# Kernel tuning notes

Hardware: AMD Instinct MI355X
Metric: run time of the kernel (lower is better)

## Reference

```python
import jax, jax.numpy as jnp
import numpy as np

N_NODES = 50000
N_EDGES = 800000
D_IN = 16
HID = 128
D_OUT = 4
N_LAYERS = 3
LN_EPS = 1e-5


def _layer_norm(h, g, b):
    mu = jnp.mean(h, axis=-1, keepdims=True)
    var = jnp.mean(jnp.square(h - mu), axis=-1, keepdims=True)
    return (h - mu) * jax.lax.rsqrt(var + LN_EPS) * g + b


def setup_inputs() -> dict:
    key = jax.random.key(0)
    ks = jax.random.split(key, 8)
    x = jax.random.normal(ks[0], (N_NODES, D_IN), jnp.float32)
    edge_index = jax.random.randint(ks[1], (2, N_EDGES), 0, N_NODES, jnp.int32)
    W_in = jax.random.normal(ks[2], (D_IN, HID), jnp.float32) / np.sqrt(D_IN)
    b_in = jnp.zeros((HID,), jnp.float32)
    Wl = jax.random.normal(ks[3], (N_LAYERS, HID, HID), jnp.float32) / np.sqrt(HID)
    bl = jnp.zeros((N_LAYERS, HID), jnp.float32)
    Wr = jax.random.normal(ks[4], (N_LAYERS, HID, HID), jnp.float32) / np.sqrt(HID)
    ln_g = jnp.ones((N_LAYERS, HID), jnp.float32)
    ln_b = jnp.zeros((N_LAYERS, HID), jnp.float32)
    W_out = jax.random.normal(ks[5], (HID, D_OUT), jnp.float32) / np.sqrt(HID)
    b_out = jnp.zeros((D_OUT,), jnp.float32)
    return {
        "x": x, "edge_index": edge_index,
        "W_in": W_in, "b_in": b_in,
        "Wl": Wl, "bl": bl, "Wr": Wr,
        "ln_g": ln_g, "ln_b": ln_b,
        "W_out": W_out, "b_out": b_out,
    }


def reference(x, edge_index, W_in, b_in, Wl, bl, Wr, ln_g, ln_b, W_out, b_out):
    # Eval mode: DropEdge and dropout are identity.
    src, dst = edge_index[0], edge_index[1]
    n = x.shape[0]
    e = edge_index.shape[1]
    # Mean-aggregation normalizer over incoming edges (PyG SAGEConv aggr='mean').
    deg = jax.ops.segment_sum(jnp.ones((e,), x.dtype), dst, num_segments=n)
    inv_deg = 1.0 / jnp.maximum(deg, 1.0)  # [N]

    h = x @ W_in + b_in  # [N, HID]
    for i in range(N_LAYERS):
        hn = _layer_norm(h, ln_g[i], ln_b[i])
        # gather source features [E, HID], scatter-sum into destinations, then mean
        agg = jax.ops.segment_sum(hn[src], dst, num_segments=n) * inv_deg[:, None]
        conv = agg @ Wl[i] + bl[i] + hn @ Wr[i]  # lin_l(mean) + lin_r(self)
        h = jax.nn.relu(h + conv)  # residual + relu
    return h @ W_out + b_out  # [N, D_OUT]
```

## Files before the change

kernel.cpp:

```cpp
#include <hip/hip_runtime.h>

#define N_NODES 50000
#define N_EDGES 800000
#define D_IN 16
#define HID 128
#define D_OUT 4
#define N_LAYERS 3
#define LN_EPS 1e-5f
#define ELL_CAP 48
#define NBUCK 196
#define BCAP 5120
#define SENT N_NODES
#define NBP 256
#define EPB (N_EDGES / NBP)
#define NB_W    (N_LAYERS * 128)
#define NB_IN   (N_NODES / 16)

typedef __attribute__((ext_vector_type(8))) short bf16x8;
typedef __attribute__((ext_vector_type(4))) float f32x4;
typedef __attribute__((ext_vector_type(2))) float f32x2;

__device__ __forceinline__ unsigned short f2bf(float f) {
    union { float f; unsigned int u; } a; a.f = f;
    unsigned int r = a.u + 0x7fffu + ((a.u >> 16) & 1u);
    return (unsigned short)(r >> 16);
}
__device__ __forceinline__ unsigned int pack2(float x, float y) {
    return (unsigned int)f2bf(x) | ((unsigned int)f2bf(y) << 16);
}
__device__ __forceinline__ float bf2f(unsigned short u) {
    union { unsigned int u; float f; } c; c.u = (unsigned int)u << 16; return c.f;
}

__global__ __launch_bounds__(256) void prep_kernel(
        const int* __restrict__ src, const int* __restrict__ dst,
        int* __restrict__ gbase, unsigned int* __restrict__ part,
        const float* __restrict__ Wl, const float* __restrict__ Wr,
        unsigned short* __restrict__ BT,
        const float* __restrict__ x, const float* __restrict__ W_in,
        const float* __restrict__ b_in,
        const float* __restrict__ g0, const float* __restrict__ bb0,
        unsigned short* __restrict__ h, unsigned short* __restrict__ hnb,
        unsigned char* __restrict__ a8) {
    __shared__ int cnt[NBUCK];
    int b = blockIdx.x, t = threadIdx.x;
    if (b < NBP) {
        if (t < NBUCK) cnt[t] = 0;
        __syncthreads();
        int e0 = b * EPB;
        for (int i = t; i < EPB; i += 256)
            atomicAdd(&cnt[dst[e0 + i] >> 8], 1);
        __syncthreads();
        int mybase = 0;
        if (t < NBUCK) mybase = atomicAdd(&gbase[t], cnt[t]);
        __syncthreads();
        if (t < NBUCK) cnt[t] = mybase;
        __syncthreads();
        for (int i = t; i < EPB; i += 256) {
            int d = dst[e0 + i];
            int bk = d >> 8;
            int pos = atomicAdd(&cnt[bk], 1);
            if (pos < BCAP)
                part[(size_t)bk * BCAP + pos] =
                    (unsigned int)src[e0 + i] | ((unsigned int)(d & 255) << 16);
        }
        return;
    }
    b -= NBP;
    if (b < NB_W) {
        int i = b >> 7, n = b & 127;
        float v = (t < 128) ? Wl[((size_t)i * 128 + t) * 128 + n]
                            : Wr[((size_t)i * 128 + (t - 128)) * 128 + n];
        BT[((size_t)i * 128 + n) * 256 + t] = f2bf(v);
        return;
    }
    b -= NB_W;
    int l = t & 15, nq = t >> 4;
    int node = b * 16 + nq;
    if (node >= N_NODES) return;
    int qb = (t & 63) & ~15;
    int j0 = l * 8;
    float xv = x[(size_t)node * D_IN + l];
    float acc[8];
    {
        float4 b0 = *(const float4*)(b_in + j0);
        float4 b1 = *(const float4*)(b_in + j0 + 4);
        acc[0] = b0.x; acc[1] = b0.y; acc[2] = b0.z; acc[3] = b0.w;
        acc[4] = b1.x; acc[5] = b1.y; acc[6] = b1.z; acc[7] = b1.w;
    }
    #pragma unroll
    for (int k = 0; k < D_IN; ++k) {
        float xk = __shfl(xv, qb + k, 64);
        float4 w0 = *(const float4*)(W_in + k * HID + j0);
        float4 w1 = *(const float4*)(W_in + k * HID + j0 + 4);
        acc[0] += xk * w0.x; acc[1] += xk * w0.y; acc[2] += xk * w0.z; acc[3] += xk * w0.w;
        acc[4] += xk * w1.x; acc[5] += xk * w1.y; acc[6] += xk * w1.z; acc[7] += xk * w1.w;
    }
    unsigned int hw[4];
    hw[0] = pack2(acc[0], acc[1]); hw[1] = pack2(acc[2], acc[3]);
    hw[2] = pack2(acc[4], acc[5]); hw[3] = pack2(acc[6], acc[7]);
    ((uint4*)h)[(size_t)node * 16 + l] = *(uint4*)hw;
    float s = ((acc[0] + acc[1]) + (acc[2] + acc[3])) + ((acc[4] + acc[5]) + (acc[6] + acc[7]));
    #pragma unroll
    for (int o = 1; o < 16; o <<= 1) s += __shfl_xor(s, o, 64);
    float mu = s * (1.0f / HID);
    float qs = 0.f;
    float d[8];
    #pragma unroll
    for (int j = 0; j < 8; ++j) { d[j] = acc[j] - mu; qs += d[j] * d[j]; }
    #pragma unroll
    for (int o = 1; o < 16; o <<= 1) qs += __shfl_xor(qs, o, 64);
    float rstd = rsqrtf(qs * (1.0f / HID) + LN_EPS);
    float4 gv0 = *(const float4*)(g0 + j0), gv1 = *(const float4*)(g0 + j0 + 4);
    float4 bv0 = *(const float4*)(bb0 + j0), bv1 = *(const float4*)(bb0 + j0 + 4);
    float hv[8];
    hv[0] = d[0] * rstd * gv0.x + bv0.x; hv[1] = d[1] * rstd * gv0.y + bv0.y;
    hv[2] = d[2] * rstd * gv0.z + bv0.z; hv[3] = d[3] * rstd * gv0.w + bv0.w;
    hv[4] = d[4] * rstd * gv1.x + bv1.x; hv[5] = d[5] * rstd * gv1.y + bv1.y;
    hv[6] = d[6] * rstd * gv1.z + bv1.z; hv[7] = d[7] * rstd * gv1.w + bv1.w;
    unsigned int nw[4];
    nw[0] = pack2(hv[0], hv[1]); nw[1] = pack2(hv[2], hv[3]);
    nw[2] = pack2(hv[4], hv[5]); nw[3] = pack2(hv[6], hv[7]);
    ((uint4*)hnb)[(size_t)node * 16 + l] = *(uint4*)nw;
    int r0 = __builtin_amdgcn_cvt_pk_fp8_f32(hv[0], hv[1], 0, false);
    r0     = __builtin_amdgcn_cvt_pk_fp8_f32(hv[2], hv[3], r0, true);
    int r1 = __builtin_amdgcn_cvt_pk_fp8_f32(hv[4], hv[5], 0, false);
    r1     = __builtin_amdgcn_cvt_pk_fp8_f32(hv[6], hv[7], r1, true);
    uint2 o8; o8.x = (unsigned int)r0; o8.y = (unsigned int)r1;
    *(uint2*)(a8 + (size_t)node * 256 + 128 + (size_t)l * 8) = o8;
}

__global__ __launch_bounds__(256) void ell_kernel(
        const unsigned int* __restrict__ part, const int* __restrict__ gbase,
        unsigned short* __restrict__ ell, int* __restrict__ cursor,
        unsigned char* __restrict__ a8) {
    __shared__ int cnt[256];
    int b = blockIdx.x, t = threadIdx.x;
    cnt[t] = 0;
    __syncthreads();
    int total = gbase[b];
    if (total > BCAP) total = BCAP;
    int n0 = b * 256;
    for (int i = t; i < total; i += 256) {
        unsigned int rec = part[(size_t)b * BCAP + i];
        int dl = rec >> 16;
        int slot = atomicAdd(&cnt[dl], 1);
        if (slot < ELL_CAP)
            ell[(size_t)(n0 + dl) * ELL_CAP + slot] = (unsigned short)(rec & 0xffff);
    }
    __syncthreads();
    int n = n0 + t;
    if (n < N_NODES) {
        int c = cnt[t];
        cursor[n] = c;
        int cap = c < ELL_CAP ? c : ELL_CAP;
        int padto = (cap + 7) & ~7;
        for (int s2 = cap; s2 < padto; ++s2)
            ell[(size_t)n * ELL_CAP + s2] = (unsigned short)SENT;
    }
    if (b == 0 && t < 32)
        ((unsigned int*)(a8 + (size_t)SENT * 256 + 128))[t] = 0u;
}

__global__ __launch_bounds__(256) void gather_kernel(
        const int* __restrict__ cursor, const unsigned short* __restrict__ ell,
        unsigned char* __restrict__ a8) {
    int tid = threadIdx.x;
    int node = blockIdx.x * 16 + (tid >> 4);
    if (node >= N_NODES) return;
    int l = tid & 15;
    int qbase = (tid & 63) & ~15;
    const uint2* base = (const uint2*)a8;
    const unsigned short* row = ell + (size_t)node * ELL_CAP;
    int cnt = cursor[node];
    int mc = cnt < ELL_CAP ? cnt : ELL_CAP;
    int mp = (mc + 7) & ~7;
    float a[8];
    #pragma unroll
    for (int j = 0; j < 8; ++j) a[j] = 0.f;
    for (int i = 0; i < mp; i += 8) {
        int sv = row[i + (l & 7)];
        uint2 vv[8];
        #pragma unroll
        for (int j = 0; j < 8; ++j) {
            int s = __shfl(sv, qbase + j, 64);
            vv[j] = base[(size_t)s * 32 + 16 + l];
        }
        #pragma unroll
        for (int j = 0; j < 8; ++j) {
            f32x2 p0 = __builtin_amdgcn_cvt_pk_f32_fp8((int)vv[j].x, false);
            f32x2 p1 = __builtin_amdgcn_cvt_pk_f32_fp8((int)vv[j].x, true);
            f32x2 p2 = __builtin_amdgcn_cvt_pk_f32_fp8((int)vv[j].y, false);
            f32x2 p3 = __builtin_amdgcn_cvt_pk_f32_fp8((int)vv[j].y, true);
            a[0] += p0.x; a[1] += p0.y; a[2] += p1.x; a[3] += p1.y;
            a[4] += p2.x; a[5] += p2.y; a[6] += p3.x; a[7] += p3.y;
        }
    }
    float inv = 1.0f / fmaxf((float)cnt, 1.0f);
    int r0 = __builtin_amdgcn_cvt_pk_fp8_f32(a[0] * inv, a[1] * inv, 0, false);
    r0     = __builtin_amdgcn_cvt_pk_fp8_f32(a[2] * inv, a[3] * inv, r0, true);
    int r1 = __builtin_amdgcn_cvt_pk_fp8_f32(a[4] * inv, a[5] * inv, 0, false);
    r1     = __builtin_amdgcn_cvt_pk_fp8_f32(a[6] * inv, a[7] * inv, r1, true);
    uint2 o; o.x = (unsigned int)r0; o.y = (unsigned int)r1;
    ((uint2*)a8)[(size_t)node * 32 + l] = o;
}

__global__ __launch_bounds__(256) void conv_mfma_kernel(
        const unsigned short* __restrict__ hres, const unsigned char* __restrict__ a8c,
        unsigned char* __restrict__ a8, unsigned short* __restrict__ hnb,
        const unsigned short* __restrict__ BT, const float* __restrict__ bl,
        const float* __restrict__ lng, const float* __restrict__ lnb,
        unsigned short* __restrict__ h,
        const float* __restrict__ Wout, const float* __restrict__ bout,
        float* __restrict__ out, int mode) {
    __shared__ unsigned short s_ab[2 * 128 * 64];
    unsigned short* s_a = s_ab;
    unsigned short* s_b = s_ab + 128 * 64;
    __shared__ float s_bl[128], s_g[128], s_bb[128];
    __shared__ float s_wo[512];
    __shared__ float s_bo[4];
    int tid = threadIdx.x;
    int n0 = blockIdx.x * 128;
    if (tid < 128) {
        s_bl[tid] = bl[tid];
        s_g[tid]  = (mode == 1) ? lng[tid] : 0.f;
        s_bb[tid] = (mode == 1) ? lnb[tid] : 0.f;
    }
    if (mode == 2) {
        s_wo[tid]       = Wout[tid];
        s_wo[tid + 256] = Wout[tid + 256];
        if (tid < 4) s_bo[tid] = bout[tid];
    }
    int w = tid >> 6, lane = tid & 63;
    int q = lane >> 4, c0 = lane & 15;

    f32x4 acc[2][8];
    #pragma unroll
    for (int rt = 0; rt < 2; ++rt)
        #pragma unroll
        for (int ct = 0; ct < 8; ++ct) acc[rt][ct] = (f32x4){0.f, 0.f, 0.f, 0.f};

    for (int kc = 0; kc < 4; ++kc) {
        if (kc) __syncthreads();
        if (kc < 2) {
            #pragma unroll
            for (int p = 0; p < 2; ++p) {
                int f = p * 256 + tid;
                int row = f >> 2, j = f & 3;
                uint4 v = {0u, 0u, 0u, 0u};
                int node = n0 + row;
                if (node < N_NODES)
                    v = *(const uint4*)(a8c + (size_t)node * 256 + kc * 64 + j * 16);
                f32x2 p0 = __builtin_amdgcn_cvt_pk_f32_fp8((int)v.x, false);
                f32x2 p1 = __builtin_amdgcn_cvt_pk_f32_fp8((int)v.x, true);
                f32x2 p2 = __builtin_amdgcn_cvt_pk_f32_fp8((int)v.y, false);
                f32x2 p3 = __builtin_amdgcn_cvt_pk_f32_fp8((int)v.y, true);
                uint4 o0;
                o0.x = pack2(p0.x, p0.y); o0.y = pack2(p1.x, p1.y);
                o0.z = pack2(p2.x, p2.y); o0.w = pack2(p3.x, p3.y);
                p0 = __builtin_amdgcn_cvt_pk_f32_fp8((int)v.z, false);
                p1 = __builtin_amdgcn_cvt_pk_f32_fp8((int)v.z, true);
                p2 = __builtin_amdgcn_cvt_pk_f32_fp8((int)v.w, false);
                p3 = __builtin_amdgcn_cvt_pk_f32_fp8((int)v.w, true);
                uint4 o1;
                o1.x = pack2(p0.x, p0.y); o1.y = pack2(p1.x, p1.y);
                o1.z = pack2(p2.x, p2.y); o1.w = pack2(p3.x, p3.y);
                int g0 = 2 * j, g1 = 2 * j + 1;
                *(uint4*)(s_a + row * 64 + (g0 ^ (row & 7)) * 8) = o0;
                *(uint4*)(s_a + row * 64 + (g1 ^ (row & 7)) * 8) = o1;
            }
        } else {
            #pragma unroll
            for (int p = 0; p < 4; ++p) {
                int f = p * 256 + tid;
                int row = f >> 3, g = f & 7;
                int pos = g ^ (row & 7);
                uint4 v = {0u, 0u, 0u, 0u};
                int node = n0 + row;
                if (node < N_NODES)
                    v = *(const uint4*)(hnb + (size_t)node * 128 + (kc - 2) * 64 + g * 8);
                *(uint4*)(s_a + row * 64 + pos * 8) = v;
            }
        }
        #pragma unroll
        for (int p = 0; p < 4; ++p) {
            int f = p * 256 + tid;
            int row = f >> 3, g = f & 7;
            int pos = g ^ (row & 7);
            uint4 v = *(const uint4*)(BT + (size_t)row * 256 + kc * 64 + g * 8);
            *(uint4*)(s_b + row * 64 + pos * 8) = v;
        }
        __syncthreads();
        #pragma unroll
        for (int ks = 0; ks < 2; ++ks) {
            int g = ks * 4 + q;
            bf16x8 af[2], bfr[8];
            #pragma unroll
            for (int rt = 0; rt < 2; ++rt) {
                int row = w * 32 + rt * 16 + c0;
                af[rt] = *(const bf16x8*)(s_a + row * 64 + (g ^ (row & 7)) * 8);
            }
            #pragma unroll
            for (int ct = 0; ct < 8; ++ct) {
                int row = ct * 16 + c0;
                bfr[ct] = *(const bf16x8*)(s_b + row * 64 + (g ^ (row & 7)) * 8);
            }
            #pragma unroll
            for (int rt = 0; rt < 2; ++rt)
                #pragma unroll
                for (int ct = 0; ct < 8; ++ct)
                    acc[rt][ct] = __builtin_amdgcn_mfma_f32_16x16x32_bf16(
                        af[rt], bfr[ct], acc[rt][ct], 0, 0, 0);
        }
    }

    if (mode == 1) {
        __syncthreads();
        unsigned short* s_out = s_ab;
        #pragma unroll
        for (int rt = 0; rt < 2; ++rt)
        #pragma unroll
        for (int reg = 0; reg < 4; ++reg) {
            int row = w * 32 + rt * 16 + q * 4 + reg;
            int nd = n0 + row;
            if (nd >= N_NODES) continue;
            #pragma unroll
            for (int ct = 0; ct < 8; ++ct) {
                int col = ct * 16 + c0;
                float v = acc[rt][ct][reg] + s_bl[col] + bf2f(hres[(size_t)nd * HID + col]);
                s_out[row * 128 + col] = f2bf(fmaxf(v, 0.f));
            }
        }
        __syncthreads();
        {
            int row = tid >> 1, half = tid & 1;
            if (n0 + row < N_NODES) {
                const uint4* sp = (const uint4*)s_ab + row * 16 + half * 8;
                uint4* gp = (uint4*)h + (size_t)(n0 + row) * 16 + half * 8;
                #pragma unroll
                for (int i = 0; i < 8; ++i) gp[i] = sp[i];
            }
        }
        __syncthreads();
        #pragma unroll
        for (int rt = 0; rt < 2; ++rt)
        #pragma unroll
        for (int reg = 0; reg < 4; ++reg) {
            int row = w * 32 + rt * 16 + q * 4 + reg;
            int nd = n0 + row;
            if (nd >= N_NODES) continue;
            float o2[8]; float s = 0.f;
            #pragma unroll
            for (int ct = 0; ct < 8; ++ct) {
                o2[ct] = bf2f(s_out[row * 128 + ct * 16 + c0]);
                s += o2[ct];
            }
            #pragma unroll
            for (int off = 1; off < 16; off <<= 1) s += __shfl_xor(s, off, 64);
            float mu = s * (1.0f / HID);
            float qs = 0.f;
            #pragma unroll
            for (int ct = 0; ct < 8; ++ct) { float d = o2[ct] - mu; qs += d * d; }
            #pragma unroll
            for (int off = 1; off < 16; off <<= 1) qs += __shfl_xor(qs, off, 64);
            float rstd = rsqrtf(qs * (1.0f / HID) + LN_EPS);
            #pragma unroll
            for (int ct = 0; ct < 8; ++ct) {
                int col = ct * 16 + c0;
                float hv = (o2[ct] - mu) * rstd * s_g[col] + s_bb[col];
                s_out[row * 128 + col] = f2bf(hv);
            }
        }
        __syncthreads();
        {
            int row = tid >> 1, half = tid & 1;
            if (n0 + row < N_NODES) {
                const uint4* sp = (const uint4*)s_ab + row * 16 + half * 8;
                uint4* gp = (uint4*)hnb + (size_t)(n0 + row) * 16 + half * 8;
                uint4 vv[8];
                #pragma unroll
                for (int i = 0; i < 8; ++i) { vv[i] = sp[i]; gp[i] = vv[i]; }
                unsigned int w8[16];
                #pragma unroll
                for (int i = 0; i < 8; ++i) {
                    const unsigned int* pu = (const unsigned int*)&vv[i];
                    #pragma unroll
                    for (int k2 = 0; k2 < 2; ++k2) {
                        unsigned int u0 = pu[2 * k2], u1 = pu[2 * k2 + 1];
                        int r = __builtin_amdgcn_cvt_pk_fp8_f32(
                            bf2f((unsigned short)(u0 & 0xffff)),
                            bf2f((unsigned short)(u0 >> 16)), 0, false);
                        r = __builtin_amdgcn_cvt_pk_fp8_f32(
                            bf2f((unsigned short)(u1 & 0xffff)),
                            bf2f((unsigned short)(u1 >> 16)), r, true);
                        w8[i * 2 + k2] = (unsigned int)r;
                    }
                }
                uint4* ap = (uint4*)(a8 + (size_t)(n0 + row) * 256 + 128 + half * 64);
                #pragma unroll
                for (int i = 0; i < 4; ++i) ap[i] = *(uint4*)&w8[i * 4];
            }
        }
    } else {
        #pragma unroll
        for (int rt = 0; rt < 2; ++rt) {
            #pragma unroll
            for (int reg = 0; reg < 4; ++reg) {
                int nd = n0 + w * 32 + rt * 16 + q * 4 + reg;
                if (nd >= N_NODES) continue;
                float od0 = 0.f, od1 = 0.f, od2 = 0.f, od3 = 0.f;
                #pragma unroll
                for (int ct = 0; ct < 8; ++ct) {
                    int col = ct * 16 + c0;
                    float v = acc[rt][ct][reg] + s_bl[col] + bf2f(hres[(size_t)nd * HID + col]);
                    v = fmaxf(v, 0.f);
                    od0 += v * s_wo[col * 4 + 0];
                    od1 += v * s_wo[col * 4 + 1];
                    od2 += v * s_wo[col * 4 + 2];
                    od3 += v * s_wo[col * 4 + 3];
                }
                #pragma unroll
                for (int off = 1; off < 16; off <<= 1) {
                    od0 += __shfl_xor(od0, off, 64);
                    od1 += __shfl_xor(od1, off, 64);
                    od2 += __shfl_xor(od2, off, 64);
                    od3 += __shfl_xor(od3, off, 64);
                }
                if (c0 == 0) {
                    float4 r;
                    r.x = od0 + s_bo[0]; r.y = od1 + s_bo[1];
                    r.z = od2 + s_bo[2]; r.w = od3 + s_bo[3];
                    *(float4*)(out + (size_t)nd * D_OUT) = r;
                }
            }
        }
    }
}

extern "C" void kernel_launch(void* const* d_in, const int* in_sizes, int n_in,
                              void* d_out, int out_size, void* d_ws, size_t ws_size,
                              hipStream_t stream) {
    const float* x    = (const float*)d_in[0];
    const int*   ei   = (const int*)d_in[1];
    const float* W_in = (const float*)d_in[2];
    const float* b_in = (const float*)d_in[3];
    const float* Wl   = (const float*)d_in[4];
    const float* bl   = (const float*)d_in[5];
    const float* Wr   = (const float*)d_in[6];
    const float* ln_g = (const float*)d_in[7];
    const float* ln_b = (const float*)d_in[8];
    const float* W_out= (const float*)d_in[9];
    const float* b_out= (const float*)d_in[10];
    float* out = (float*)d_out;

    unsigned short* h   = (unsigned short*)d_ws;
    unsigned short* hnb = h + (size_t)N_NODES * HID;
    unsigned short* BT  = hnb + (size_t)N_NODES * HID;
    unsigned char* a8   = (unsigned char*)(BT + (size_t)N_LAYERS * 128 * 256);
    unsigned short* ell = (unsigned short*)(a8 + (size_t)(N_NODES + 1) * 256);
    int*   cursor = (int*)(ell + (size_t)N_NODES * ELL_CAP);
    int*   gbase  = cursor + N_NODES;
    unsigned int* part = (unsigned int*)(gbase + 256);

    const int* src = ei;
    const int* dst = ei + N_EDGES;

    hipMemsetAsync(gbase, 0, 256 * sizeof(int), stream);

    prep_kernel<<<NBP + NB_W + NB_IN, 256, 0, stream>>>(
        src, dst, gbase, part, Wl, Wr, BT, x, W_in, b_in, ln_g, ln_b, h, hnb, a8);
    ell_kernel<<<NBUCK, 256, 0, stream>>>(part, gbase, ell, cursor, a8);

    for (int i = 0; i < N_LAYERS; ++i) {
        gather_kernel<<<(N_NODES + 15) / 16, 256, 0, stream>>>(cursor, ell, a8);
        int mode = (i + 1 < N_LAYERS) ? 1 : 2;
        const float* g_next = ln_g + (mode == 1 ? (size_t)(i + 1) * HID : 0);
        const float* b_next = ln_b + (mode == 1 ? (size_t)(i + 1) * HID : 0);
        conv_mfma_kernel<<<(N_NODES + 127) / 128, 256, 0, stream>>>(
            h, a8, a8, hnb, BT + (size_t)i * 128 * 256, bl + i * HID,
            g_next, b_next, h, W_out, b_out, out, mode);
    }
}
```

Baseline: 230.3 us.

## Fuse neighbor gather into conv MFMA kernel with ping-pong fp8 feature buffers

Drops the separate gather kernel. Each 128-node conv block now gathers and mean-aggregates its own nodes' neighbor features straight into LDS as bf16, where the MFMA reads them. This removes a kernel launch per layer and the fp8 round trip of the aggregate through global memory. The fp8 normalized features move to two ping-pong buffers so a layer can read the current features while writing the next. The cost is that the latency-bound random gather now runs in far fewer, LDS-heavy blocks with lower occupancy, which may hide memory latency less well.

After: 261.6 us. +13.6%, slower.

```diff
diff --git a/kernel.cpp b/kernel.cpp
--- a/kernel.cpp
+++ b/kernel.cpp
@@ -41,7 +41,7 @@
         const float* __restrict__ b_in,
         const float* __restrict__ g0, const float* __restrict__ bb0,
         unsigned short* __restrict__ h, unsigned short* __restrict__ hnb,
-        unsigned char* __restrict__ a8) {
+        unsigned char* __restrict__ hn8) {
     __shared__ int cnt[NBUCK];
     int b = blockIdx.x, t = threadIdx.x;
     if (b < NBP) {
@@ -127,13 +127,13 @@
     int r1 = __builtin_amdgcn_cvt_pk_fp8_f32(hv[4], hv[5], 0, false);
     r1     = __builtin_amdgcn_cvt_pk_fp8_f32(hv[6], hv[7], r1, true);
     uint2 o8; o8.x = (unsigned int)r0; o8.y = (unsigned int)r1;
-    *(uint2*)(a8 + (size_t)node * 256 + 128 + (size_t)l * 8) = o8;
+    *(uint2*)(hn8 + (size_t)node * 128 + (size_t)l * 8) = o8;
 }
 
 __global__ __launch_bounds__(256) void ell_kernel(
         const unsigned int* __restrict__ part, const int* __restrict__ gbase,
         unsigned short* __restrict__ ell, int* __restrict__ cursor,
-        unsigned char* __restrict__ a8) {
+        unsigned char* __restrict__ hn8a, unsigned char* __restrict__ hn8b) {
     __shared__ int cnt[256];
     int b = blockIdx.x, t = threadIdx.x;
     cnt[t] = 0;
@@ -158,64 +158,24 @@
         for (int s2 = cap; s2 < padto; ++s2)
             ell[(size_t)n * ELL_CAP + s2] = (unsigned short)SENT;
     }
-    if (b == 0 && t < 32)
-        ((unsigned int*)(a8 + (size_t)SENT * 256 + 128))[t] = 0u;
-}
-
-__global__ __launch_bounds__(256) void gather_kernel(
+    if (b == 0 && t < 32) {
+        ((unsigned int*)(hn8a + (size_t)SENT * 128))[t] = 0u;
+        ((unsigned int*)(hn8b + (size_t)SENT * 128))[t] = 0u;
+    }
+}
+
+__global__ __launch_bounds__(256) void conv_fused_kernel(
+        const unsigned short* __restrict__ hres,
         const int* __restrict__ cursor, const unsigned short* __restrict__ ell,
-        unsigned char* __restrict__ a8) {
-    int tid = threadIdx.x;
-    int node = blockIdx.x * 16 + (tid >> 4);
-    if (node >= N_NODES) return;
-    int l = tid & 15;
-    int qbase = (tid & 63) & ~15;
-    const uint2* base = (const uint2*)a8;
-    const unsigned short* row = ell + (size_t)node * ELL_CAP;
-    int cnt = cursor[node];
-    int mc = cnt < ELL_CAP ? cnt : ELL_CAP;
-    int mp = (mc + 7) & ~7;
-    float a[8];
-    #pragma unroll
-    for (int j = 0; j < 8; ++j) a[j] = 0.f;
-    for (int i = 0; i < mp; i += 8) {
-        int sv = row[i + (l & 7)];
-        uint2 vv[8];
-        #pragma unroll
-        for (int j = 0; j < 8; ++j) {
-            int s = __shfl(sv, qbase + j, 64);
-            vv[j] = base[(size_t)s * 32 + 16 + l];
-        }
-        #pragma unroll
-        for (int j = 0; j < 8; ++j) {
-            f32x2 p0 = __builtin_amdgcn_cvt_pk_f32_fp8((int)vv[j].x, false);
-            f32x2 p1 = __builtin_amdgcn_cvt_pk_f32_fp8((int)vv[j].x, true);
-            f32x2 p2 = __builtin_amdgcn_cvt_pk_f32_fp8((int)vv[j].y, false);
-            f32x2 p3 = __builtin_amdgcn_cvt_pk_f32_fp8((int)vv[j].y, true);
-            a[0] += p0.x; a[1] += p0.y; a[2] += p1.x; a[3] += p1.y;
-            a[4] += p2.x; a[5] += p2.y; a[6] += p3.x; a[7] += p3.y;
-        }
-    }
-    float inv = 1.0f / fmaxf((float)cnt, 1.0f);
-    int r0 = __builtin_amdgcn_cvt_pk_fp8_f32(a[0] * inv, a[1] * inv, 0, false);
-    r0     = __builtin_amdgcn_cvt_pk_fp8_f32(a[2] * inv, a[3] * inv, r0, true);
-    int r1 = __builtin_amdgcn_cvt_pk_fp8_f32(a[4] * inv, a[5] * inv, 0, false);
-    r1     = __builtin_amdgcn_cvt_pk_fp8_f32(a[6] * inv, a[7] * inv, r1, true);
-    uint2 o; o.x = (unsigned int)r0; o.y = (unsigned int)r1;
-    ((uint2*)a8)[(size_t)node * 32 + l] = o;
-}
-
-__global__ __launch_bounds__(256) void conv_mfma_kernel(
-        const unsigned short* __restrict__ hres, const unsigned char* __restrict__ a8c,
-        unsigned char* __restrict__ a8, unsigned short* __restrict__ hnb,
+        const unsigned char* __restrict__ hn8cur, unsigned char* __restrict__ hn8next,
+        unsigned short* __restrict__ hnb,
         const unsigned short* __restrict__ BT, const float* __restrict__ bl,
         const float* __restrict__ lng, const float* __restrict__ lnb,
         unsigned short* __restrict__ h,
         const float* __restrict__ Wout, const float* __restrict__ bout,
         float* __restrict__ out, int mode) {
-    __shared__ unsigned short s_ab[2 * 128 * 64];
-    unsigned short* s_a = s_ab;
-    unsigned short* s_b = s_ab + 128 * 64;
+    __shared__ unsigned short s_agg[2 * 128 * 64];
+    __shared__ unsigned short s_b[128 * 64];
     __shared__ float s_bl[128], s_g[128], s_bb[128];
     __shared__ float s_wo[512];
     __shared__ float s_bo[4];
@@ -234,6 +194,51 @@
     int w = tid >> 6, lane = tid & 63;
     int q = lane >> 4, c0 = lane & 15;
 
+    {
+        int qi = tid >> 4, l = tid & 15;
+        int qbase = (tid & 63) & ~15;
+        const uint2* gb = (const uint2*)hn8cur;
+        for (int j = 0; j < 8; ++j) {
+            int r = qi * 8 + j;
+            int node = n0 + r;
+            if (node < N_NODES) {
+                const unsigned short* row = ell + (size_t)node * ELL_CAP;
+                int cnt = cursor[node];
+                int mc = cnt < ELL_CAP ? cnt : ELL_CAP;
+                int mp = (mc + 7) & ~7;
+                float a[8];
+                #pragma unroll
+                for (int k2 = 0; k2 < 8; ++k2) a[k2] = 0.f;
+                for (int i = 0; i < mp; i += 8) {
+                    int sv = row[i + (l & 7)];
+                    uint2 vv[8];
+                    #pragma unroll
+                    for (int k2 = 0; k2 < 8; ++k2) {
+                        int s = __shfl(sv, qbase + k2, 64);
+                        vv[k2] = gb[(size_t)s * 16 + l];
+                    }
+                    #pragma unroll
+                    for (int k2 = 0; k2 < 8; ++k2) {
+                        f32x2 p0 = __builtin_amdgcn_cvt_pk_f32_fp8((int)vv[k2].x, false);
+                        f32x2 p1 = __builtin_amdgcn_cvt_pk_f32_fp8((int)vv[k2].x, true);
+                        f32x2 p2 = __builtin_amdgcn_cvt_pk_f32_fp8((int)vv[k2].y, false);
+                        f32x2 p3 = __builtin_amdgcn_cvt_pk_f32_fp8((int)vv[k2].y, true);
+                        a[0] += p0.x; a[1] += p0.y; a[2] += p1.x; a[3] += p1.y;
+                        a[4] += p2.x; a[5] += p2.y; a[6] += p3.x; a[7] += p3.y;
+                    }
+                }
+                float inv = 1.0f / fmaxf((float)cnt, 1.0f);
+                unsigned int wq[4];
+                wq[0] = pack2(a[0] * inv, a[1] * inv);
+                wq[1] = pack2(a[2] * inv, a[3] * inv);
+                wq[2] = pack2(a[4] * inv, a[5] * inv);
+                wq[3] = pack2(a[6] * inv, a[7] * inv);
+                int g = l & 7, half = l >> 3;
+                *(uint4*)(s_agg + half * 8192 + r * 64 + (g ^ (r & 7)) * 8) = *(uint4*)wq;
+            }
+        }
+    }
+
     f32x4 acc[2][8];
     #pragma unroll
     for (int rt = 0; rt < 2; ++rt)
@@ -241,35 +246,8 @@
         for (int ct = 0; ct < 8; ++ct) acc[rt][ct] = (f32x4){0.f, 0.f, 0.f, 0.f};
 
     for (int kc = 0; kc < 4; ++kc) {
-        if (kc) __syncthreads();
-        if (kc < 2) {
-            #pragma unroll
-            for (int p = 0; p < 2; ++p) {
-                int f = p * 256 + tid;
-                int row = f >> 2, j = f & 3;
-                uint4 v = {0u, 0u, 0u, 0u};
-                int node = n0 + row;
-                if (node < N_NODES)
-                    v = *(const uint4*)(a8c + (size_t)node * 256 + kc * 64 + j * 16);
-                f32x2 p0 = __builtin_amdgcn_cvt_pk_f32_fp8((int)v.x, false);
-                f32x2 p1 = __builtin_amdgcn_cvt_pk_f32_fp8((int)v.x, true);
-                f32x2 p2 = __builtin_amdgcn_cvt_pk_f32_fp8((int)v.y, false);
-                f32x2 p3 = __builtin_amdgcn_cvt_pk_f32_fp8((int)v.y, true);
-                uint4 o0;
-                o0.x = pack2(p0.x, p0.y); o0.y = pack2(p1.x, p1.y);
-                o0.z = pack2(p2.x, p2.y); o0.w = pack2(p3.x, p3.y);
-                p0 = __builtin_amdgcn_cvt_pk_f32_fp8((int)v.z, false);
-                p1 = __builtin_amdgcn_cvt_pk_f32_fp8((int)v.z, true);
-                p2 = __builtin_amdgcn_cvt_pk_f32_fp8((int)v.w, false);
-                p3 = __builtin_amdgcn_cvt_pk_f32_fp8((int)v.w, true);
-                uint4 o1;
-                o1.x = pack2(p0.x, p0.y); o1.y = pack2(p1.x, p1.y);
-                o1.z = pack2(p2.x, p2.y); o1.w = pack2(p3.x, p3.y);
-                int g0 = 2 * j, g1 = 2 * j + 1;
-                *(uint4*)(s_a + row * 64 + (g0 ^ (row & 7)) * 8) = o0;
-                *(uint4*)(s_a + row * 64 + (g1 ^ (row & 7)) * 8) = o1;
-            }
-        } else {
+        __syncthreads();
+        if (kc >= 2) {
             #pragma unroll
             for (int p = 0; p < 4; ++p) {
                 int f = p * 256 + tid;
@@ -279,7 +257,7 @@
                 int node = n0 + row;
                 if (node < N_NODES)
                     v = *(const uint4*)(hnb + (size_t)node * 128 + (kc - 2) * 64 + g * 8);
-                *(uint4*)(s_a + row * 64 + pos * 8) = v;
+                *(uint4*)(s_agg + (kc - 2) * 8192 + row * 64 + pos * 8) = v;
             }
         }
         #pragma unroll
@@ -291,6 +269,7 @@
             *(uint4*)(s_b + row * 64 + pos * 8) = v;
         }
         __syncthreads();
+        const unsigned short* s_a = s_agg + (kc & 1) * 8192;
         #pragma unroll
         for (int ks = 0; ks < 2; ++ks) {
             int g = ks * 4 + q;
@@ -316,7 +295,7 @@
 
     if (mode == 1) {
         __syncthreads();
-        unsigned short* s_out = s_ab;
+        unsigned short* s_out = s_agg;
         #pragma unroll
         for (int rt = 0; rt < 2; ++rt)
         #pragma unroll
@@ -335,7 +314,7 @@
         {
             int row = tid >> 1, half = tid & 1;
             if (n0 + row < N_NODES) {
-                const uint4* sp = (const uint4*)s_ab + row * 16 + half * 8;
+                const uint4* sp = (const uint4*)s_out + row * 16 + half * 8;
                 uint4* gp = (uint4*)h + (size_t)(n0 + row) * 16 + half * 8;
                 #pragma unroll
                 for (int i = 0; i < 8; ++i) gp[i] = sp[i];
@@ -375,7 +354,7 @@
         {
             int row = tid >> 1, half = tid & 1;
             if (n0 + row < N_NODES) {
-                const uint4* sp = (const uint4*)s_ab + row * 16 + half * 8;
+                const uint4* sp = (const uint4*)s_out + row * 16 + half * 8;
                 uint4* gp = (uint4*)hnb + (size_t)(n0 + row) * 16 + half * 8;
                 uint4 vv[8];
                 #pragma unroll
@@ -396,7 +375,7 @@
                         w8[i * 2 + k2] = (unsigned int)r;
                     }
                 }
-                uint4* ap = (uint4*)(a8 + (size_t)(n0 + row) * 256 + 128 + half * 64);
+                uint4* ap = (uint4*)(hn8next + (size_t)(n0 + row) * 128 + half * 64);
                 #pragma unroll
                 for (int i = 0; i < 4; ++i) ap[i] = *(uint4*)&w8[i * 4];
             }
@@ -456,8 +435,9 @@
     unsigned short* h   = (unsigned short*)d_ws;
     unsigned short* hnb = h + (size_t)N_NODES * HID;
     unsigned short* BT  = hnb + (size_t)N_NODES * HID;
-    unsigned char* a8   = (unsigned char*)(BT + (size_t)N_LAYERS * 128 * 256);
-    unsigned short* ell = (unsigned short*)(a8 + (size_t)(N_NODES + 1) * 256);
+    unsigned char* hn8a = (unsigned char*)(BT + (size_t)N_LAYERS * 128 * 256);
+    unsigned char* hn8b = hn8a + (size_t)(N_NODES + 1) * 128;
+    unsigned short* ell = (unsigned short*)(hn8b + (size_t)(N_NODES + 1) * 128);
     int*   cursor = (int*)(ell + (size_t)N_NODES * ELL_CAP);
     int*   gbase  = cursor + N_NODES;
     unsigned int* part = (unsigned int*)(gbase + 256);
@@ -468,16 +448,18 @@
     hipMemsetAsync(gbase, 0, 256 * sizeof(int), stream);
 
     prep_kernel<<<NBP + NB_W + NB_IN, 256, 0, stream>>>(
-        src, dst, gbase, part, Wl, Wr, BT, x, W_in, b_in, ln_g, ln_b, h, hnb, a8);
-    ell_kernel<<<NBUCK, 256, 0, stream>>>(part, gbase, ell, cursor, a8);
-
+        src, dst, gbase, part, Wl, Wr, BT, x, W_in, b_in, ln_g, ln_b, h, hnb, hn8a);
+    ell_kernel<<<NBUCK, 256, 0, stream>>>(part, gbase, ell, cursor, hn8a, hn8b);
+
+    unsigned char* cur8 = hn8a;
+    unsigned char* nxt8 = hn8b;
     for (int i = 0; i < N_LAYERS; ++i) {
-        gather_kernel<<<(N_NODES + 15) / 16, 256, 0, stream>>>(cursor, ell, a8);
         int mode = (i + 1 < N_LAYERS) ? 1 : 2;
         const float* g_next = ln_g + (mode == 1 ? (size_t)(i + 1) * HID : 0);
         const float* b_next = ln_b + (mode == 1 ? (size_t)(i + 1) * HID : 0);
-        conv_mfma_kernel<<<(N_NODES + 127) / 128, 256, 0, stream>>>(
-            h, a8, a8, hnb, BT + (size_t)i * 128 * 256, bl + i * HID,
+        conv_fused_kernel<<<(N_NODES + 127) / 128, 256, 0, stream>>>(
+            h, cursor, ell, cur8, nxt8, hnb, BT + (size_t)i * 128 * 256, bl + i * HID,
             g_next, b_next, h, W_out, b_out, out, mode);
-    }
-}
+        unsigned char* t2 = cur8; cur8 = nxt8; nxt8 = t2;
+    }
+}
```
